# Kernel optimization log

Measured on AMD Instinct MI355X. Metric: run time of the kernel, lower is better.

The kernel has to match this reference:

```python
import jax, jax.numpy as jnp
import numpy as np

N, E, D, H, LAYERS = 50000, 800000, 128, 8, 2
LRELU_ALPHA = 0.2


def _seg_softmax(logits, seg, n):
    # numerically stable softmax over edges grouped by destination node
    m = jax.ops.segment_max(logits, seg, num_segments=n)
    z = jnp.exp(logits - m[seg])
    s = jax.ops.segment_sum(z, seg, num_segments=n)
    return z / jnp.maximum(s[seg], 1e-16)


def _gat_layer(x, src, dst, W, a_src, a_dst, concat):
    # W: [H, Fin, F'], a_src/a_dst: [H, F']
    n = x.shape[0]
    outs = []
    for h in range(W.shape[0]):  # loop over heads to bound peak memory
        Wh = x @ W[h]                              # [N, F']
        es = Wh @ a_src[h]                         # [N]
        ed = Wh @ a_dst[h]                         # [N]
        e = jax.nn.leaky_relu(es[src] + ed[dst], LRELU_ALPHA)  # [E]
        att = _seg_softmax(e, dst, n)              # [E]
        out = jax.ops.segment_sum(att[:, None] * Wh[src], dst, num_segments=n)
        outs.append(out)
    if concat:
        return jax.nn.elu(jnp.concatenate(outs, axis=-1))  # [N, H*F']
    return jnp.mean(jnp.stack(outs, axis=0), axis=0)        # [N, F']


def _rel_gcn_layer(x, src, dst, w, W):
    # weighted-adjacency GCN with row (in-degree) normalization + ReLU
    n = x.shape[0]
    deg = jax.ops.segment_sum(w, dst, num_segments=n)
    norm = w / jnp.maximum(deg[dst], 1e-16)        # [E]
    h = x @ W                                      # [N, Dout]
    agg = jax.ops.segment_sum(norm[:, None] * h[src], dst, num_segments=n)
    return jax.nn.relu(agg)


def setup_inputs() -> dict:
    key = jax.random.key(0)
    ks = jax.random.split(key, 12)
    s = 1.0 / np.sqrt(D)
    return {
        "x": jax.random.normal(ks[0], (N, D), dtype=jnp.float32),
        "edge_index": jax.random.randint(ks[1], (2, E), 0, N, dtype=jnp.int64),
        "edge_weight": jax.random.uniform(ks[2], (E,), dtype=jnp.float32),
        "gat_W0": jax.random.normal(ks[3], (H, D, D // H), dtype=jnp.float32) * s,
        "gat_a0_src": jax.random.normal(ks[4], (H, D // H), dtype=jnp.float32) * s,
        "gat_a0_dst": jax.random.normal(ks[5], (H, D // H), dtype=jnp.float32) * s,
        "gat_W1": jax.random.normal(ks[6], (H, D, D), dtype=jnp.float32) * s,
        "gat_a1_src": jax.random.normal(ks[7], (H, D), dtype=jnp.float32) * s,
        "gat_a1_dst": jax.random.normal(ks[8], (H, D), dtype=jnp.float32) * s,
        "gcn_W0": jax.random.normal(ks[9], (D, D), dtype=jnp.float32) * s,
        "gcn_W1": jax.random.normal(ks[10], (D, D), dtype=jnp.float32) * s,
    }


def reference(x, edge_index, edge_weight, gat_W0, gat_a0_src, gat_a0_dst,
              gat_W1, gat_a1_src, gat_a1_dst, gcn_W0, gcn_W1):
    src, dst = edge_index[0], edge_index[1]
    gat_params = [(gat_W0, gat_a0_src, gat_a0_dst), (gat_W1, gat_a1_src, gat_a1_dst)]
    gcn_params = [gcn_W0, gcn_W1]
    x1, x2 = x, x  # dropout is identity in eval mode
    for i in range(LAYERS):
        W, a_s, a_d = gat_params[i]
        x1 = _gat_layer(x1, src, dst, W, a_s, a_d, concat=(i != LAYERS - 1))
        x2 = _rel_gcn_layer(x2, src, dst, edge_weight, gcn_params[i])
    # cat along new last dim then MaxPool1d(2) == elementwise max of branches
    return jnp.maximum(x1, x2)
```

## Files before the change

kernel.cpp:

```cpp
#include <hip/hip_runtime.h>

#define LRELU_ALPHA 0.2f

typedef __attribute__((ext_vector_type(8))) short short8;
typedef __attribute__((ext_vector_type(4))) float float4v;
typedef __attribute__((ext_vector_type(2))) float f32x2;

__device__ __forceinline__ unsigned short f2bf(float f) {
  union { float f; unsigned u; } x; x.f = f;
  unsigned r = (x.u + 0x7fff + ((x.u >> 16) & 1)) >> 16;
  return (unsigned short)r;
}
__device__ __forceinline__ float bflo(unsigned u) {
  union { unsigned u; float f; } x; x.u = u << 16; return x.f;
}
__device__ __forceinline__ float bfhi(unsigned u) {
  union { unsigned u; float f; } x; x.u = u & 0xffff0000u; return x.f;
}
__device__ __forceinline__ f32x2 bfpair(unsigned u) {
  return (f32x2){bflo(u), bfhi(u)};
}
__device__ __forceinline__ unsigned packbf(float a, float b) {
  return (unsigned)f2bf(a) | ((unsigned)f2bf(b) << 16);
}


__global__ __launch_bounds__(256) void k_count(const int* __restrict__ dst,
                                               int* __restrict__ cnt, int E) {
  int e = blockIdx.x * 256 + threadIdx.x;
  if (e < E) atomicAdd(&cnt[dst[e]], 1);
}

__global__ __launch_bounds__(1024) void k_scan1(const int* __restrict__ cnt,
                                                int* __restrict__ lscan,
                                                int* __restrict__ bsum, int N) {
  __shared__ int ws[16];
  int t = threadIdx.x, lane = t & 63, wid = t >> 6;
  int i = blockIdx.x * 1024 + t;
  int v = (i < N) ? cnt[i] : 0;
  int orig = v;
#pragma unroll
  for (int off = 1; off < 64; off <<= 1) {
    int y = __shfl_up(v, off, 64);
    if (lane >= off) v += y;
  }
  if (lane == 63) ws[wid] = v;
  __syncthreads();
  if (t < 16) {
    int s = ws[t], o = s;
#pragma unroll
    for (int off = 1; off < 16; off <<= 1) {
      int y = __shfl_up(s, off, 16);
      if (t >= off) s += y;
    }
    ws[t] = s - o;
  }
  __syncthreads();
  if (i < N) lscan[i] = ws[wid] + v - orig;
  if (t == 1023) bsum[blockIdx.x] = ws[15] + v;
}

__global__ __launch_bounds__(64) void k_scan2(int* __restrict__ bsum,
                                              int* __restrict__ rowptrN, int nb) {
  int t = threadIdx.x;
  int v = (t < nb) ? bsum[t] : 0;
  int orig = v;
  for (int off = 1; off < 64; off <<= 1) {
    int y = __shfl_up(v, off, 64);
    if (t >= off) v += y;
  }
  if (t < nb) bsum[t] = v - orig;
  if (t == 63) *rowptrN = v;
}

__global__ __launch_bounds__(1024) void k_scan3(int* __restrict__ rowptr,
                                                int* __restrict__ cur,
                                                const int* __restrict__ bsum, int N) {
  int i = blockIdx.x * 1024 + threadIdx.x;
  if (i < N) {
    int v = rowptr[i] + bsum[blockIdx.x];
    rowptr[i] = v;
    cur[i] = v;
  }
}

__global__ __launch_bounds__(256) void k_scatter(const int* __restrict__ src,
                                                 const int* __restrict__ dst,
                                                 const float* __restrict__ w,
                                                 const float* __restrict__ logit0,
                                                 int* __restrict__ cur,
                                                 uint2* __restrict__ edata,
                                                 unsigned short* __restrict__ pedge,
                                                 int E) {
  int base = (blockIdx.x * 256 + threadIdx.x) * 4;
  if (base >= E) return;
  int n = E - base; if (n > 4) n = 4;
  int ss[4], dd[4]; float ww[4];
  if (n == 4) {
    int4 s4 = *(const int4*)(src + base);
    int4 d4 = *(const int4*)(dst + base);
    float4 w4 = *(const float4*)(w + base);
    ss[0] = s4.x; ss[1] = s4.y; ss[2] = s4.z; ss[3] = s4.w;
    dd[0] = d4.x; dd[1] = d4.y; dd[2] = d4.z; dd[3] = d4.w;
    ww[0] = w4.x; ww[1] = w4.y; ww[2] = w4.z; ww[3] = w4.w;
  } else {
    for (int i = 0; i < n; ++i) { ss[i] = src[base + i]; dd[i] = dst[base + i]; ww[i] = w[base + i]; }
  }
  int pp[4];
#pragma unroll
  for (int i = 0; i < 4; ++i)
    if (i < n) pp[i] = atomicAdd(&cur[dd[i]], 1);
#pragma unroll
  for (int i = 0; i < 4; ++i) {
    if (i >= n) break;
    int s = ss[i], d = dd[i], p = pp[i];
    edata[p] = make_uint2((unsigned)s, __float_as_uint(ww[i]));
    float4 es0 = *(const float4*)(logit0 + (size_t)s * 16);
    float4 es1 = *(const float4*)(logit0 + (size_t)s * 16 + 4);
    float4 ed0 = *(const float4*)(logit0 + (size_t)d * 16 + 8);
    float4 ed1 = *(const float4*)(logit0 + (size_t)d * 16 + 12);
    float lg[8] = {es0.x + ed0.x, es0.y + ed0.y, es0.z + ed0.z, es0.w + ed0.w,
                   es1.x + ed1.x, es1.y + ed1.y, es1.z + ed1.z, es1.w + ed1.w};
    unsigned short o[8];
#pragma unroll
    for (int h = 0; h < 8; ++h) {
      float v = lg[h] > 0.f ? lg[h] : LRELU_ALPHA * lg[h];
      o[h] = f2bf(__expf(fminf(v, 80.f)));
    }
    ushort4 q0 = {o[0], o[1], o[2], o[3]};
    ushort4 q1 = {o[4], o[5], o[6], o[7]};
    *(ushort4*)(pedge + (size_t)p * 8) = q0;
    *(ushort4*)(pedge + (size_t)p * 8 + 4) = q1;
  }
}

__global__ __launch_bounds__(256) void k_pack(const float* __restrict__ W0,
                                              const float* __restrict__ a0s,
                                              const float* __restrict__ a0d,
                                              const float* __restrict__ W1,
                                              const float* __restrict__ a1s,
                                              const float* __restrict__ a1d,
                                              const float* __restrict__ gw0,
                                              const float* __restrict__ gw1,
                                              unsigned short* __restrict__ W0catT,
                                              float* __restrict__ logitW,
                                              unsigned short* __restrict__ gw1T,
                                              unsigned short* __restrict__ va1T,
                                              unsigned short* __restrict__ WstackT) {
  int idx = blockIdx.x * 256 + threadIdx.x;
  if (idx < 32768) {
    int n = idx >> 7, k = idx & 127;
    float v;
    if (n < 128) {
      int h = n >> 4, f = n & 15;
      v = W0[h * 2048 + k * 16 + f];
    } else {
      v = gw0[k * 128 + (n - 128)];
    }
    W0catT[idx] = f2bf(v);
  } else if (idx < 34816) {
    int j = idx - 32768;
    int k = j >> 4, c = j & 15;
    int h = (c < 8) ? c : c - 8;
    const float* a = (c < 8) ? a0s : a0d;
    float s = 0.f;
    for (int f = 0; f < 16; ++f) s += W0[h * 2048 + k * 16 + f] * a[h * 16 + f];
    logitW[j] = s;
  } else if (idx < 51200) {
    int j = idx - 34816;
    int n = j >> 7, k = j & 127;
    gw1T[j] = f2bf(gw1[k * 128 + n]);
  } else if (idx < 53248) {
    int j = idx - 51200;
    int c = j >> 7, k = j & 127;
    int h = c & 7;
    const float* a = (c < 8) ? a1s : a1d;
    float s = 0.f;
    for (int f = 0; f < 128; ++f) s += W1[h * 16384 + k * 128 + f] * a[h * 128 + f];
    va1T[j] = f2bf(s);
  } else if (idx < 184320) {
    int j = idx - 53248;
    int n = j >> 10, kk = j & 1023;
    int h = kk >> 7, k = kk & 127;
    WstackT[j] = f2bf(W1[h * 16384 + k * 128 + n] * 0.125f);
  }
}

__global__ __launch_bounds__(256) void k_prep(const float* __restrict__ x,
                                              const float* __restrict__ logitW,
                                              unsigned short* __restrict__ xb,
                                              float* __restrict__ logit0, int N) {
  __shared__ float sm[16][132];
  __shared__ float sw[2048];
  int t = threadIdx.x;
  int base = blockIdx.x * 16;
  int r = t >> 4, cc = (t & 15) * 8;
  const float* xr = x + (size_t)(base + r) * 128 + cc;
  float4 v0 = *(const float4*)xr;
  float4 v1 = *(const float4*)(xr + 4);
  ushort4 o0 = {f2bf(v0.x), f2bf(v0.y), f2bf(v0.z), f2bf(v0.w)};
  ushort4 o1 = {f2bf(v1.x), f2bf(v1.y), f2bf(v1.z), f2bf(v1.w)};
  *(ushort4*)(xb + (size_t)(base + r) * 128 + cc) = o0;
  *(ushort4*)(xb + (size_t)(base + r) * 128 + cc + 4) = o1;
  *(float4*)&sm[r][cc] = v0;
  *(float4*)&sm[r][cc + 4] = v1;
  *(float4*)&sw[t * 8] = *(const float4*)(logitW + t * 8);
  *(float4*)&sw[t * 8 + 4] = *(const float4*)(logitW + t * 8 + 4);
  __syncthreads();
  int c = t & 15;
  float acc = 0.f;
#pragma unroll
  for (int k = 0; k < 128; ++k) acc += sm[r][k] * sw[k * 16 + c];
  logit0[(size_t)(base + r) * 16 + c] = acc;
}

__global__ __launch_bounds__(256) void k_pedge(const float* __restrict__ logits,
                                               const uint2* __restrict__ edata,
                                               const int* __restrict__ rowptr,
                                               unsigned short* __restrict__ pedge,
                                               float* __restrict__ linv, int N) {
  int wave = threadIdx.x >> 6, lane = threadIdx.x & 63;
  int d = blockIdx.x * 4 + wave;
  if (d >= N) return;
  int j8 = lane >> 3, h = lane & 7;
  float edv = logits[(size_t)d * 16 + 8 + h];
  int beg = rowptr[d], end = rowptr[d + 1];
  float lsum = 0.f;
  for (int ii = beg + j8; ii < end; ii += 8) {
    unsigned s = edata[ii].x;
    float es = logits[(size_t)s * 16 + h];
    float lg = es + edv;
    lg = lg > 0.f ? lg : LRELU_ALPHA * lg;
    float p = __expf(fminf(lg, 80.f));
    lsum += p;
    pedge[(size_t)ii * 8 + h] = f2bf(p);
  }
  lsum += __shfl_xor(lsum, 8, 64);
  lsum += __shfl_xor(lsum, 16, 64);
  lsum += __shfl_xor(lsum, 32, 64);
  if (lane < 8) linv[(size_t)d * 8 + h] = lsum > 0.f ? 1.f / lsum : 0.f;
}

template <int NT, int OUT_BF16, int EPI>
__global__ __launch_bounds__(256) void k_mgemm(const unsigned short* __restrict__ A, int lda,
                                               const unsigned short* __restrict__ BT, int ldb,
                                               void* __restrict__ Cv, int ldc,
                                               const void* __restrict__ aux,
                                               int M, int Ncols, int K) {
  __shared__ unsigned short As[64][64];
  __shared__ unsigned short Bs[NT * 16][64];
  int tid = threadIdx.x;
  int w = tid >> 6, lane = tid & 63;
  int quad = lane >> 4, l16 = lane & 15;
  int row0 = blockIdx.x * 64;
  int c0 = blockIdx.y * (NT * 16);
  float4v acc[NT];
#pragma unroll
  for (int t = 0; t < NT; ++t) acc[t] = (float4v){0.f, 0.f, 0.f, 0.f};

  for (int k0 = 0; k0 < K; k0 += 64) {
    __syncthreads();
#pragma unroll
    for (int i = 0; i < 2; ++i) {
      int c = tid + i * 256;
      int r = c >> 3, kc = c & 7;
      uint4 v = {0u, 0u, 0u, 0u};
      int gr = row0 + r;
      if (gr < M) v = *(const uint4*)(A + (size_t)gr * lda + k0 + kc * 8);
      *(uint4*)(&As[r][(kc ^ (r & 7)) * 8]) = v;
    }
#pragma unroll
    for (int i = 0; i < (NT * 128 + 255) / 256; ++i) {
      int c = tid + i * 256;
      if (c < NT * 128) {
        int n = c >> 3, kc = c & 7;
        uint4 v = {0u, 0u, 0u, 0u};
        int gn = c0 + n;
        if (gn < Ncols) v = *(const uint4*)(BT + (size_t)gn * ldb + k0 + kc * 8);
        *(uint4*)(&Bs[n][(kc ^ (n & 7)) * 8]) = v;
      }
    }
    __syncthreads();
#pragma unroll
    for (int ks = 0; ks < 2; ++ks) {
      int m = w * 16 + l16;
      int ga = (ks * 4 + quad) ^ (m & 7);
      short8 a = *(const short8*)(&As[m][ga * 8]);
#pragma unroll
      for (int t = 0; t < NT; ++t) {
        int n = t * 16 + l16;
        int gb = (ks * 4 + quad) ^ (n & 7);
        short8 b = *(const short8*)(&Bs[n][gb * 8]);
        acc[t] = __builtin_amdgcn_mfma_f32_16x16x32_bf16(a, b, acc[t], 0, 0, 0);
      }
    }
  }
#pragma unroll
  for (int t = 0; t < NT; ++t) {
    int cc = c0 + t * 16 + l16;
    if (cc >= Ncols) continue;
#pragma unroll
    for (int i = 0; i < 4; ++i) {
      int rr = row0 + w * 16 + quad * 4 + i;
      if (rr >= M) continue;
      float v = acc[t][i];
      if (EPI == 1) {
        unsigned short us = ((const unsigned short*)aux)[(size_t)rr * ldc + cc];
        v = fmaxf(v, bflo((unsigned)us));
      }
      if (EPI == 5) v = fmaxf(v, 0.f);
      if (EPI == 4) {
        if (cc < 128) {
          ((unsigned short*)Cv)[(size_t)rr * 192 + cc] = f2bf(v);
        } else {
          int enc = __builtin_amdgcn_cvt_pk_fp8_f32(v, v, 0, false);
          ((unsigned char*)aux)[(size_t)rr * 384 + 256 + (cc - 128)] = (unsigned char)(enc & 0xff);
        }
      } else if (OUT_BF16)
        ((unsigned short*)Cv)[(size_t)rr * ldc + cc] = f2bf(v);
      else
        ((float*)Cv)[(size_t)rr * ldc + cc] = v;
    }
  }
}

__global__ __launch_bounds__(256, 8) void k_agg0(const unsigned short* __restrict__ feat,
                                                 const int* __restrict__ rowptr,
                                                 const uint2* __restrict__ edata,
                                                 const unsigned short* __restrict__ pedge,
                                                 unsigned short* __restrict__ xh,
                                                 unsigned short* __restrict__ x1cc, int N) {
  __shared__ uint2 swl[4][64];
  __shared__ float pl[4][512];
  int wave = threadIdx.x >> 6, lane = threadIdx.x & 63;
  int head = lane >> 3;
  const char* FG = (const char*)feat + lane * 4;
  const char* FC = (const char*)feat + 256 + lane * 2;
  for (int d = blockIdx.x * 4 + wave; d < N; d += gridDim.x * 4) {
    int beg = rowptr[d], end = rowptr[d + 1], deg = end - beg;
    f32x2 aa = {0.f, 0.f}, ga = {0.f, 0.f};
    float l = 0.f, wsum = 0.f;
    for (int base = 0; base < deg; base += 64) {
      int idx = beg + base + lane;
      uint2 sv = make_uint2(0u, 0u);
      uint4 q = make_uint4(0u, 0u, 0u, 0u);
      if (idx < end) {
        sv = edata[idx];
        q = *(const uint4*)(pedge + (size_t)idx * 8);
      }
      swl[wave][lane] = sv;
      float4 pa = make_float4(bflo(q.x), bfhi(q.x), bflo(q.y), bfhi(q.y));
      float4 pb = make_float4(bflo(q.z), bfhi(q.z), bflo(q.w), bfhi(q.w));
      *(float4*)&pl[wave][lane * 8] = pa;
      *(float4*)&pl[wave][lane * 8 + 4] = pb;
      int ng = deg - base; if (ng > 64) ng = 64;
      int t = 0;
      for (; t + 4 <= ng; t += 4) {
        uint2 s0 = swl[wave][t], s1 = swl[wave][t + 1];
        uint2 s2 = swl[wave][t + 2], s3 = swl[wave][t + 3];
        unsigned g0 = *(const unsigned*)(FG + (size_t)s0.x * 384);
        unsigned g1 = *(const unsigned*)(FG + (size_t)s1.x * 384);
        unsigned g2 = *(const unsigned*)(FG + (size_t)s2.x * 384);
        unsigned g3 = *(const unsigned*)(FG + (size_t)s3.x * 384);
        unsigned c0 = *(const unsigned short*)(FC + (size_t)s0.x * 384);
        unsigned c1 = *(const unsigned short*)(FC + (size_t)s1.x * 384);
        unsigned c2 = *(const unsigned short*)(FC + (size_t)s2.x * 384);
        unsigned c3 = *(const unsigned short*)(FC + (size_t)s3.x * 384);
        float p0 = pl[wave][t * 8 + head];
        float p1 = pl[wave][t * 8 + 8 + head];
        float p2 = pl[wave][t * 8 + 16 + head];
        float p3 = pl[wave][t * 8 + 24 + head];
        float w0 = __uint_as_float(s0.y), w1 = __uint_as_float(s1.y);
        float w2 = __uint_as_float(s2.y), w3 = __uint_as_float(s3.y);
        aa += bfpair(g0) * p0; ga += __builtin_amdgcn_cvt_pk_f32_fp8(c0, false) * w0;
        l += p0; wsum += w0;
        aa += bfpair(g1) * p1; ga += __builtin_amdgcn_cvt_pk_f32_fp8(c1, false) * w1;
        l += p1; wsum += w1;
        aa += bfpair(g2) * p2; ga += __builtin_amdgcn_cvt_pk_f32_fp8(c2, false) * w2;
        l += p2; wsum += w2;
        aa += bfpair(g3) * p3; ga += __builtin_amdgcn_cvt_pk_f32_fp8(c3, false) * w3;
        l += p3; wsum += w3;
      }
      for (; t < ng; ++t) {
        uint2 s0 = swl[wave][t];
        unsigned g0 = *(const unsigned*)(FG + (size_t)s0.x * 384);
        unsigned c0 = *(const unsigned short*)(FC + (size_t)s0.x * 384);
        float p0 = pl[wave][t * 8 + head];
        float w0 = __uint_as_float(s0.y);
        aa += bfpair(g0) * p0; ga += __builtin_amdgcn_cvt_pk_f32_fp8(c0, false) * w0;
        l += p0; wsum += w0;
      }
    }
    float inv = l > 0.f ? 1.f / l : 0.f;
    float v0 = aa.x * inv, v1 = aa.y * inv;
    v0 = v0 > 0.f ? v0 : __expf(v0) - 1.f;
    v1 = v1 > 0.f ? v1 : __expf(v1) - 1.f;
    float ginv = 1.f / fmaxf(wsum, 1e-16f);
    unsigned px = packbf(v0, v1);
    ((uint2*)xh)[(size_t)d * 64 + lane] =
        make_uint2(px, packbf(fmaxf(ga.x * ginv, 0.f), fmaxf(ga.y * ginv, 0.f)));
    ((unsigned*)x1cc)[(size_t)d * 64 + lane] = px;
  }
}

__global__ __launch_bounds__(256, 8) void k_agg1(const unsigned short* __restrict__ xh,
                                                 const int* __restrict__ rowptr,
                                                 const uint2* __restrict__ edata,
                                                 const unsigned short* __restrict__ pedge,
                                                 const float* __restrict__ linv,
                                                 unsigned short* __restrict__ aggbuf,
                                                 unsigned short* __restrict__ x2a, int N) {
  __shared__ uint2 swl[4][64];
  __shared__ float pl[4][512];
  int wave = threadIdx.x >> 6, lane = threadIdx.x & 63;
  const uint2* X2 = (const uint2*)xh + lane;
  for (int d = blockIdx.x * 4 + wave; d < N; d += gridDim.x * 4) {
    int beg = rowptr[d], end = rowptr[d + 1], deg = end - beg;
    f32x2 axp[8] = {};
    f32x2 gp = {0.f, 0.f};
    float wsum = 0.f;
#define EDGE1(uu, ss, tt)                                    \
  {                                                          \
    float4 pv0 = *(const float4*)&pl[wave][(tt) * 8];        \
    float4 pv1 = *(const float4*)&pl[wave][(tt) * 8 + 4];    \
    float wj = __uint_as_float((ss).y);                      \
    f32x2 xA = bfpair((uu).x);                               \
    f32x2 hA = bfpair((uu).y);                               \
    axp[0] += xA * pv0.x; axp[1] += xA * pv0.y;              \
    axp[2] += xA * pv0.z; axp[3] += xA * pv0.w;              \
    axp[4] += xA * pv1.x; axp[5] += xA * pv1.y;              \
    axp[6] += xA * pv1.z; axp[7] += xA * pv1.w;              \
    gp += hA * wj; wsum += wj;                               \
  }
    for (int base = 0; base < deg; base += 64) {
      int idx = beg + base + lane;
      uint2 sv = make_uint2(0u, 0u);
      uint4 q = make_uint4(0u, 0u, 0u, 0u);
      if (idx < end) {
        sv = edata[idx];
        q = *(const uint4*)(pedge + (size_t)idx * 8);
      }
      swl[wave][lane] = sv;
      float4 pa = make_float4(bflo(q.x), bfhi(q.x), bflo(q.y), bfhi(q.y));
      float4 pb = make_float4(bflo(q.z), bfhi(q.z), bflo(q.w), bfhi(q.w));
      *(float4*)&pl[wave][lane * 8] = pa;
      *(float4*)&pl[wave][lane * 8 + 4] = pb;
      int ng = deg - base; if (ng > 64) ng = 64;
      int t = 0;
      for (; t + 4 <= ng; t += 4) {
        uint2 s0 = swl[wave][t], s1 = swl[wave][t + 1];
        uint2 s2 = swl[wave][t + 2], s3 = swl[wave][t + 3];
        uint2 u0 = X2[(size_t)s0.x * 64];
        uint2 u1 = X2[(size_t)s1.x * 64];
        uint2 u2 = X2[(size_t)s2.x * 64];
        uint2 u3 = X2[(size_t)s3.x * 64];
        EDGE1(u0, s0, t)
        EDGE1(u1, s1, t + 1)
        EDGE1(u2, s2, t + 2)
        EDGE1(u3, s3, t + 3)
      }
      for (; t < ng; ++t) {
        uint2 s0 = swl[wave][t];
        uint2 u0 = X2[(size_t)s0.x * 64];
        EDGE1(u0, s0, t)
      }
    }
#undef EDGE1
    float4 i0 = *(const float4*)(linv + (size_t)d * 8);
    float4 i1 = *(const float4*)(linv + (size_t)d * 8 + 4);
    unsigned* ab = (unsigned*)aggbuf + (size_t)d * 512 + lane;
    ab[0]   = packbf(axp[0].x * i0.x, axp[0].y * i0.x);
    ab[64]  = packbf(axp[1].x * i0.y, axp[1].y * i0.y);
    ab[128] = packbf(axp[2].x * i0.z, axp[2].y * i0.z);
    ab[192] = packbf(axp[3].x * i0.w, axp[3].y * i0.w);
    ab[256] = packbf(axp[4].x * i1.x, axp[4].y * i1.x);
    ab[320] = packbf(axp[5].x * i1.y, axp[5].y * i1.y);
    ab[384] = packbf(axp[6].x * i1.z, axp[6].y * i1.z);
    ab[448] = packbf(axp[7].x * i1.w, axp[7].y * i1.w);
    float ginv = 1.f / fmaxf(wsum, 1e-16f);
    ((unsigned*)x2a)[(size_t)d * 64 + lane] = packbf(gp.x * ginv, gp.y * ginv);
  }
}


extern "C" void kernel_launch(void* const* d_in, const int* in_sizes, int n_in,
                              void* d_out, int out_size, void* d_ws, size_t ws_size,
                              hipStream_t stream) {
  const float* x   = (const float*)d_in[0];
  const int*   ei  = (const int*)d_in[1];
  const float* ew  = (const float*)d_in[2];
  const float* W0  = (const float*)d_in[3];
  const float* a0s = (const float*)d_in[4];
  const float* a0d = (const float*)d_in[5];
  const float* W1  = (const float*)d_in[6];
  const float* a1s = (const float*)d_in[7];
  const float* a1d = (const float*)d_in[8];
  const float* gw0 = (const float*)d_in[9];
  const float* gw1 = (const float*)d_in[10];
  float* out = (float*)d_out;

  const int N = in_sizes[0] / 128;
  const int E = in_sizes[1] / 2;
  const int* src = ei;
  const int* dst = ei + E;

  char* p = (char*)d_ws;
  auto carve = [&](size_t bytes) {
    void* r = (void*)p;
    p += (bytes + 255) & ~(size_t)255;
    return r;
  };
  int*   cnt    = (int*)carve((size_t)N * 4);
  int*   rowptr = (int*)carve((size_t)(N + 1) * 4);
  int*   cur    = (int*)carve((size_t)N * 4);
  int*   bsum   = (int*)carve(256 * 4);
  uint2* edata  = (uint2*)carve((size_t)E * 8);
  unsigned short* W0catT  = (unsigned short*)carve(32768 * 2);
  float*          logitW  = (float*)carve(2048 * 4);
  unsigned short* gw1T    = (unsigned short*)carve(16384 * 2);
  unsigned short* va1T    = (unsigned short*)carve(2048 * 2);
  unsigned short* WstackT = (unsigned short*)carve(131072 * 2);
  float*          esed = (float*)carve((size_t)N * 16 * 4);
  unsigned short* xh   = (unsigned short*)carve((size_t)N * 512);
  unsigned short* x2a  = (unsigned short*)carve((size_t)N * 128 * 2);
  unsigned short* pedge = (unsigned short*)carve((size_t)E * 8 * 2);
  float*          linv  = (float*)carve((size_t)N * 8 * 4);
  size_t ph1 = ((size_t)N * 128 * 2 + 255) & ~(size_t)255;
  size_t ph2 = ph1 + (((size_t)N * 384 + 255) & ~(size_t)255);
  size_t ph3 = ph2 + (((size_t)N * 16 * 4 + 255) & ~(size_t)255);
  size_t scratch_sz = (size_t)N * 1024 * 2;
  if (ph3 > scratch_sz) scratch_sz = ph3;
  char* scratch = (char*)carve(scratch_sz);
  unsigned short* xb     = (unsigned short*)scratch;
  unsigned short* x1cc   = (unsigned short*)scratch;
  unsigned short* feat   = (unsigned short*)(scratch + ph1);
  float*          logit0 = (float*)(scratch + ph2);
  unsigned short* aggbuf = (unsigned short*)scratch;

  int gE = (E + 255) / 256;
  int gE4 = ((E + 3) / 4 + 255) / 256;
  int nb = (N + 1023) / 1024;
  int gM = (N + 63) / 64;
  int gD = (N + 3) / 4;
  int gA = gD < 2048 ? gD : 2048;

  hipMemsetAsync(cnt, 0, (size_t)N * 4, stream);
  k_count<<<gE, 256, 0, stream>>>(dst, cnt, E);
  k_scan1<<<nb, 1024, 0, stream>>>(cnt, rowptr, bsum, N);
  k_scan2<<<1, 64, 0, stream>>>(bsum, rowptr + N, nb);
  k_scan3<<<nb, 1024, 0, stream>>>(rowptr, cur, bsum, N);

  k_pack<<<(184320 + 255) / 256, 256, 0, stream>>>(W0, a0s, a0d, W1, a1s, a1d, gw0,
                                                   gw1, W0catT, logitW, gw1T, va1T,
                                                   WstackT);
  k_prep<<<(N + 15) / 16, 256, 0, stream>>>(x, logitW, xb, logit0, N);

  k_scatter<<<gE4, 256, 0, stream>>>(src, dst, ew, logit0, cur, edata, pedge, E);

  k_mgemm<8, 1, 4><<<dim3(gM, 2), 256, 0, stream>>>(xb, 128, W0catT, 128, feat, 192,
                                                    feat, N, 256, 128);
  k_agg0<<<gA, 256, 0, stream>>>(feat, rowptr, edata, pedge, xh, x1cc, N);

  k_mgemm<1, 0, 0><<<dim3(gM, 1), 256, 0, stream>>>(x1cc, 128, va1T, 128, esed, 16,
                                                    nullptr, N, 16, 128);

  k_pedge<<<gD, 256, 0, stream>>>(esed, edata, rowptr, pedge, linv, N);

  k_agg1<<<gA, 256, 0, stream>>>(xh, rowptr, edata, pedge, linv, aggbuf, x2a, N);

  k_mgemm<8, 1, 5><<<dim3(gM, 1), 256, 0, stream>>>(x2a, 128, gw1T, 128, x2a, 128,
                                                    nullptr, N, 128, 128);

  k_mgemm<8, 0, 1><<<dim3(gM, 1), 256, 0, stream>>>(aggbuf, 1024, WstackT, 1024, out,
                                                    128, x2a, N, 128, 1024);
}
```

Measured before the change: 449.1 us.

## Compute layer-0 attention weights inside aggregation instead of precomputing per edge

The scatter kernel no longer computes and stores per-edge bf16 exp(leaky_relu) weights for layer 0. Instead the source-side logits are packed into the feature row, now widened from 384 to 448 bytes, and k_agg0 recomputes the exponentials on the fly. This removes a 16 B per-edge write and read plus the LDS staging, in exchange for extra exp math in the aggregation and a wider gathered row. Scatter can now launch before k_pack/k_prep because it no longer depends on logit0.

```diff
diff --git a/kernel.cpp b/kernel.cpp
--- a/kernel.cpp
+++ b/kernel.cpp
@@ -87,11 +87,8 @@
 __global__ __launch_bounds__(256) void k_scatter(const int* __restrict__ src,
                                                  const int* __restrict__ dst,
                                                  const float* __restrict__ w,
-                                                 const float* __restrict__ logit0,
                                                  int* __restrict__ cur,
-                                                 uint2* __restrict__ edata,
-                                                 unsigned short* __restrict__ pedge,
-                                                 int E) {
+                                                 uint2* __restrict__ edata, int E) {
   int base = (blockIdx.x * 256 + threadIdx.x) * 4;
   if (base >= E) return;
   int n = E - base; if (n > 4) n = 4;
@@ -111,27 +108,8 @@
   for (int i = 0; i < 4; ++i)
     if (i < n) pp[i] = atomicAdd(&cur[dd[i]], 1);
 #pragma unroll
-  for (int i = 0; i < 4; ++i) {
-    if (i >= n) break;
-    int s = ss[i], d = dd[i], p = pp[i];
-    edata[p] = make_uint2((unsigned)s, __float_as_uint(ww[i]));
-    float4 es0 = *(const float4*)(logit0 + (size_t)s * 16);
-    float4 es1 = *(const float4*)(logit0 + (size_t)s * 16 + 4);
-    float4 ed0 = *(const float4*)(logit0 + (size_t)d * 16 + 8);
-    float4 ed1 = *(const float4*)(logit0 + (size_t)d * 16 + 12);
-    float lg[8] = {es0.x + ed0.x, es0.y + ed0.y, es0.z + ed0.z, es0.w + ed0.w,
-                   es1.x + ed1.x, es1.y + ed1.y, es1.z + ed1.z, es1.w + ed1.w};
-    unsigned short o[8];
-#pragma unroll
-    for (int h = 0; h < 8; ++h) {
-      float v = lg[h] > 0.f ? lg[h] : LRELU_ALPHA * lg[h];
-      o[h] = f2bf(__expf(fminf(v, 80.f)));
-    }
-    ushort4 q0 = {o[0], o[1], o[2], o[3]};
-    ushort4 q1 = {o[4], o[5], o[6], o[7]};
-    *(ushort4*)(pedge + (size_t)p * 8) = q0;
-    *(ushort4*)(pedge + (size_t)p * 8 + 4) = q1;
-  }
+  for (int i = 0; i < 4; ++i)
+    if (i < n) edata[pp[i]] = make_uint2((unsigned)ss[i], __float_as_uint(ww[i]));
 }
 
 __global__ __launch_bounds__(256) void k_pack(const float* __restrict__ W0,
@@ -189,7 +167,8 @@
 __global__ __launch_bounds__(256) void k_prep(const float* __restrict__ x,
                                               const float* __restrict__ logitW,
                                               unsigned short* __restrict__ xb,
-                                              float* __restrict__ logit0, int N) {
+                                              float* __restrict__ logit0,
+                                              char* __restrict__ feat, int N) {
   __shared__ float sm[16][132];
   __shared__ float sw[2048];
   int t = threadIdx.x;
@@ -212,6 +191,8 @@
 #pragma unroll
   for (int k = 0; k < 128; ++k) acc += sm[r][k] * sw[k * 16 + c];
   logit0[(size_t)(base + r) * 16 + c] = acc;
+  if (c < 8)
+    *(float*)(feat + (size_t)(base + r) * 448 + 384 + c * 4) = acc;
 }
 
 __global__ __launch_bounds__(256) void k_pedge(const float* __restrict__ logits,
@@ -311,10 +292,10 @@
       if (EPI == 5) v = fmaxf(v, 0.f);
       if (EPI == 4) {
         if (cc < 128) {
-          ((unsigned short*)Cv)[(size_t)rr * 192 + cc] = f2bf(v);
+          ((unsigned short*)Cv)[(size_t)rr * 224 + cc] = f2bf(v);
         } else {
           int enc = __builtin_amdgcn_cvt_pk_fp8_f32(v, v, 0, false);
-          ((unsigned char*)aux)[(size_t)rr * 384 + 256 + (cc - 128)] = (unsigned char)(enc & 0xff);
+          ((unsigned char*)aux)[(size_t)rr * 448 + 256 + (cc - 128)] = (unsigned char)(enc & 0xff);
         }
       } else if (OUT_BF16)
         ((unsigned short*)Cv)[(size_t)rr * ldc + cc] = f2bf(v);
@@ -327,51 +308,57 @@
 __global__ __launch_bounds__(256, 8) void k_agg0(const unsigned short* __restrict__ feat,
                                                  const int* __restrict__ rowptr,
                                                  const uint2* __restrict__ edata,
-                                                 const unsigned short* __restrict__ pedge,
+                                                 const float* __restrict__ logit0,
                                                  unsigned short* __restrict__ xh,
                                                  unsigned short* __restrict__ x1cc, int N) {
   __shared__ uint2 swl[4][64];
-  __shared__ float pl[4][512];
   int wave = threadIdx.x >> 6, lane = threadIdx.x & 63;
   int head = lane >> 3;
-  const char* FG = (const char*)feat + lane * 4;
-  const char* FC = (const char*)feat + 256 + lane * 2;
+  const char* F = (const char*)feat;
+  int goff = lane * 4;
+  int coff = 256 + lane * 2;
+  int eoff = 384 + head * 4;
   for (int d = blockIdx.x * 4 + wave; d < N; d += gridDim.x * 4) {
     int beg = rowptr[d], end = rowptr[d + 1], deg = end - beg;
+    float edv = logit0[(size_t)d * 16 + 8 + head];
     f32x2 aa = {0.f, 0.f}, ga = {0.f, 0.f};
     float l = 0.f, wsum = 0.f;
     for (int base = 0; base < deg; base += 64) {
       int idx = beg + base + lane;
       uint2 sv = make_uint2(0u, 0u);
-      uint4 q = make_uint4(0u, 0u, 0u, 0u);
-      if (idx < end) {
-        sv = edata[idx];
-        q = *(const uint4*)(pedge + (size_t)idx * 8);
-      }
+      if (idx < end) sv = edata[idx];
       swl[wave][lane] = sv;
-      float4 pa = make_float4(bflo(q.x), bfhi(q.x), bflo(q.y), bfhi(q.y));
-      float4 pb = make_float4(bflo(q.z), bfhi(q.z), bflo(q.w), bfhi(q.w));
-      *(float4*)&pl[wave][lane * 8] = pa;
-      *(float4*)&pl[wave][lane * 8 + 4] = pb;
       int ng = deg - base; if (ng > 64) ng = 64;
       int t = 0;
       for (; t + 4 <= ng; t += 4) {
         uint2 s0 = swl[wave][t], s1 = swl[wave][t + 1];
         uint2 s2 = swl[wave][t + 2], s3 = swl[wave][t + 3];
-        unsigned g0 = *(const unsigned*)(FG + (size_t)s0.x * 384);
-        unsigned g1 = *(const unsigned*)(FG + (size_t)s1.x * 384);
-        unsigned g2 = *(const unsigned*)(FG + (size_t)s2.x * 384);
-        unsigned g3 = *(const unsigned*)(FG + (size_t)s3.x * 384);
-        unsigned c0 = *(const unsigned short*)(FC + (size_t)s0.x * 384);
-        unsigned c1 = *(const unsigned short*)(FC + (size_t)s1.x * 384);
-        unsigned c2 = *(const unsigned short*)(FC + (size_t)s2.x * 384);
-        unsigned c3 = *(const unsigned short*)(FC + (size_t)s3.x * 384);
-        float p0 = pl[wave][t * 8 + head];
-        float p1 = pl[wave][t * 8 + 8 + head];
-        float p2 = pl[wave][t * 8 + 16 + head];
-        float p3 = pl[wave][t * 8 + 24 + head];
+        const char* r0 = F + (size_t)s0.x * 448;
+        const char* r1 = F + (size_t)s1.x * 448;
+        const char* r2 = F + (size_t)s2.x * 448;
+        const char* r3 = F + (size_t)s3.x * 448;
+        unsigned g0 = *(const unsigned*)(r0 + goff);
+        unsigned g1 = *(const unsigned*)(r1 + goff);
+        unsigned g2 = *(const unsigned*)(r2 + goff);
+        unsigned g3 = *(const unsigned*)(r3 + goff);
+        unsigned c0 = *(const unsigned short*)(r0 + coff);
+        unsigned c1 = *(const unsigned short*)(r1 + coff);
+        unsigned c2 = *(const unsigned short*)(r2 + coff);
+        unsigned c3 = *(const unsigned short*)(r3 + coff);
+        float e0 = *(const float*)(r0 + eoff);
+        float e1 = *(const float*)(r1 + eoff);
+        float e2 = *(const float*)(r2 + eoff);
+        float e3 = *(const float*)(r3 + eoff);
         float w0 = __uint_as_float(s0.y), w1 = __uint_as_float(s1.y);
         float w2 = __uint_as_float(s2.y), w3 = __uint_as_float(s3.y);
+        float lg0 = e0 + edv; lg0 = lg0 > 0.f ? lg0 : LRELU_ALPHA * lg0;
+        float lg1 = e1 + edv; lg1 = lg1 > 0.f ? lg1 : LRELU_ALPHA * lg1;
+        float lg2 = e2 + edv; lg2 = lg2 > 0.f ? lg2 : LRELU_ALPHA * lg2;
+        float lg3 = e3 + edv; lg3 = lg3 > 0.f ? lg3 : LRELU_ALPHA * lg3;
+        float p0 = __expf(fminf(lg0, 80.f));
+        float p1 = __expf(fminf(lg1, 80.f));
+        float p2 = __expf(fminf(lg2, 80.f));
+        float p3 = __expf(fminf(lg3, 80.f));
         aa += bfpair(g0) * p0; ga += __builtin_amdgcn_cvt_pk_f32_fp8(c0, false) * w0;
         l += p0; wsum += w0;
         aa += bfpair(g1) * p1; ga += __builtin_amdgcn_cvt_pk_f32_fp8(c1, false) * w1;
@@ -383,10 +370,13 @@
       }
       for (; t < ng; ++t) {
         uint2 s0 = swl[wave][t];
-        unsigned g0 = *(const unsigned*)(FG + (size_t)s0.x * 384);
-        unsigned c0 = *(const unsigned short*)(FC + (size_t)s0.x * 384);
-        float p0 = pl[wave][t * 8 + head];
+        const char* r0 = F + (size_t)s0.x * 448;
+        unsigned g0 = *(const unsigned*)(r0 + goff);
+        unsigned c0 = *(const unsigned short*)(r0 + coff);
+        float e0 = *(const float*)(r0 + eoff);
         float w0 = __uint_as_float(s0.y);
+        float lg0 = e0 + edv; lg0 = lg0 > 0.f ? lg0 : LRELU_ALPHA * lg0;
+        float p0 = __expf(fminf(lg0, 80.f));
         aa += bfpair(g0) * p0; ga += __builtin_amdgcn_cvt_pk_f32_fp8(c0, false) * w0;
         l += p0; wsum += w0;
       }
@@ -526,7 +516,7 @@
   unsigned short* pedge = (unsigned short*)carve((size_t)E * 8 * 2);
   float*          linv  = (float*)carve((size_t)N * 8 * 4);
   size_t ph1 = ((size_t)N * 128 * 2 + 255) & ~(size_t)255;
-  size_t ph2 = ph1 + (((size_t)N * 384 + 255) & ~(size_t)255);
+  size_t ph2 = ph1 + (((size_t)N * 448 + 255) & ~(size_t)255);
   size_t ph3 = ph2 + (((size_t)N * 16 * 4 + 255) & ~(size_t)255);
   size_t scratch_sz = (size_t)N * 1024 * 2;
   if (ph3 > scratch_sz) scratch_sz = ph3;
@@ -550,16 +540,16 @@
   k_scan2<<<1, 64, 0, stream>>>(bsum, rowptr + N, nb);
   k_scan3<<<nb, 1024, 0, stream>>>(rowptr, cur, bsum, N);
 
+  k_scatter<<<gE4, 256, 0, stream>>>(src, dst, ew, cur, edata, E);
+
   k_pack<<<(184320 + 255) / 256, 256, 0, stream>>>(W0, a0s, a0d, W1, a1s, a1d, gw0,
                                                    gw1, W0catT, logitW, gw1T, va1T,
                                                    WstackT);
-  k_prep<<<(N + 15) / 16, 256, 0, stream>>>(x, logitW, xb, logit0, N);
-
-  k_scatter<<<gE4, 256, 0, stream>>>(src, dst, ew, logit0, cur, edata, pedge, E);
-
-  k_mgemm<8, 1, 4><<<dim3(gM, 2), 256, 0, stream>>>(xb, 128, W0catT, 128, feat, 192,
+  k_prep<<<(N + 15) / 16, 256, 0, stream>>>(x, logitW, xb, logit0, (char*)feat, N);
+
+  k_mgemm<8, 1, 4><<<dim3(gM, 2), 256, 0, stream>>>(xb, 128, W0catT, 128, feat, 224,
                                                     feat, N, 256, 128);
-  k_agg0<<<gA, 256, 0, stream>>>(feat, rowptr, edata, pedge, xh, x1cc, N);
+  k_agg0<<<gA, 256, 0, stream>>>(feat, rowptr, edata, logit0, xh, x1cc, N);
 
   k_mgemm<1, 0, 0><<<dim3(gM, 1), 256, 0, stream>>>(x1cc, 128, va1T, 128, esed, 16,
                                                     nullptr, N, 16, 128);
```

Result: no change. 453.6 us (+1.0%).
